# Optimization experiments

Hardware: AMD Instinct MI355X
Metric: run time of the kernel (lower is better)

## Reference

```python
import jax, jax.numpy as jnp
import numpy as np

LOG_CLAMP = -100.0  # torch.nn.BCELoss clamps log terms at -100


def setup_inputs() -> dict:
    key = jax.random.key(0)
    k1, k2 = jax.random.split(key)
    shape = (64, 8, 65536, 1)  # [B, C, H, W]
    vertical_pred = jax.random.uniform(k1, shape, dtype=jnp.float32)
    vertical_true = jax.random.uniform(k2, shape, dtype=jnp.float32)
    return {"vertical_pred": vertical_pred, "vertical_true": vertical_true}


def reference(vertical_pred, vertical_true):
    # Only the first width column is used: [B, C, H]
    p = vertical_pred[..., 0]
    t = vertical_true[..., 0]
    log_p = jnp.clip(jnp.log(p), LOG_CLAMP)
    log_1mp = jnp.clip(jnp.log1p(-p), LOG_CLAMP)
    bce = -(t * log_p + (1.0 - t) * log_1mp)           # [B, C, H]
    per_bc = jnp.mean(bce, axis=-1)                     # mean over H per (b, c)
    loss = jnp.sum(per_bc) / vertical_pred.shape[0]     # sum over b,c then / B
    return loss
```

## Files before the change

kernel.cpp:

```cpp
#include <hip/hip_runtime.h>


#define LOG2_CLAMP -144.26950408889634f

typedef float vfloat4 __attribute__((ext_vector_type(4)));

__device__ __forceinline__ void bce4_acc(vfloat4 p, vfloat4 t,
                                         float& sq, float& sd) {
    float lp, lq;
    lp = fmaxf(__log2f(p.x), LOG2_CLAMP);
    lq = fmaxf(__log2f(1.0f - p.x), LOG2_CLAMP);
    sq += lq; sd = __builtin_fmaf(t.x, lp - lq, sd);
    lp = fmaxf(__log2f(p.y), LOG2_CLAMP);
    lq = fmaxf(__log2f(1.0f - p.y), LOG2_CLAMP);
    sq += lq; sd = __builtin_fmaf(t.y, lp - lq, sd);
    lp = fmaxf(__log2f(p.z), LOG2_CLAMP);
    lq = fmaxf(__log2f(1.0f - p.z), LOG2_CLAMP);
    sq += lq; sd = __builtin_fmaf(t.z, lp - lq, sd);
    lp = fmaxf(__log2f(p.w), LOG2_CLAMP);
    lq = fmaxf(__log2f(1.0f - p.w), LOG2_CLAMP);
    sq += lq; sd = __builtin_fmaf(t.w, lp - lq, sd);
}

__global__ __launch_bounds__(256) void vertical_loss_kernel(
    const vfloat4* __restrict__ p4,
    const vfloat4* __restrict__ t4,
    float* __restrict__ out,
    int n4, float final_scale)
{
    float sq = 0.0f, sd = 0.0f;

    const int chunk = n4 / (int)gridDim.x;
    const int steps = chunk / (int)blockDim.x;

    if ((chunk % (int)blockDim.x) == 0 && steps > 0) {
        const int stp = (int)blockDim.x;
        int i = (int)blockIdx.x * chunk + (int)threadIdx.x;
        #pragma unroll 4
        for (int s = 0; s < steps; ++s, i += stp) {
            vfloat4 p = __builtin_nontemporal_load(&p4[i]);
            vfloat4 t = __builtin_nontemporal_load(&t4[i]);
            bce4_acc(p, t, sq, sd);
        }
    } else {
        for (int i = (int)blockIdx.x * (int)blockDim.x + (int)threadIdx.x;
             i < n4; i += (int)gridDim.x * (int)blockDim.x) {
            vfloat4 p = __builtin_nontemporal_load(&p4[i]);
            vfloat4 t = __builtin_nontemporal_load(&t4[i]);
            bce4_acc(p, t, sq, sd);
        }
    }

    float sum = sq + sd;

    #pragma unroll
    for (int off = 32; off > 0; off >>= 1)
        sum += __shfl_down(sum, off, 64);

    __shared__ float wsum[4];
    int wave = threadIdx.x >> 6;
    int lane = threadIdx.x & 63;
    if (lane == 0) wsum[wave] = sum;
    __syncthreads();

    if (threadIdx.x == 0) {
        float s = wsum[0] + wsum[1] + wsum[2] + wsum[3];
        atomicAdd(out, s * final_scale);
    }
}

extern "C" void kernel_launch(void* const* d_in, const int* in_sizes, int n_in,
                              void* d_out, int out_size, void* d_ws, size_t ws_size,
                              hipStream_t stream) {
    const vfloat4* pred  = (const vfloat4*)d_in[0];
    const vfloat4* true_ = (const vfloat4*)d_in[1];
    float* out = (float*)d_out;

    int n  = in_sizes[0];
    int n4 = n / 4;
    float final_scale = -0.69314718055994531f / (65536.0f * 64.0f);

    (void)hipMemsetAsync(d_out, 0, sizeof(float), stream);

    int blocks = 2048;
    vertical_loss_kernel<<<blocks, 256, 0, stream>>>(pred, true_, out, n4, final_scale);
}
```

Baseline: 254.5 us.

## Software-pipeline loads with inline asm cache-bypass global loads and explicit waitcnt

Replaces the unrolled nontemporal-load loop with a hand-written double-buffered pipeline. Each iteration issues inline-asm global_load_dwordx4 with sc0 sc1 nt cache-bypass bits and uses explicit s_waitcnt plus sched barriers, so two iterations of loads stay in flight while the math runs. The aim is better memory-level parallelism and less cache pollution on a purely bandwidth-bound stream. In exchange, it may keep fewer loads outstanding than the compiler's unroll-by-4, and the unsigned 32-bit byte offsets limit how large the inputs can be.

```diff
diff --git a/kernel.cpp b/kernel.cpp
--- a/kernel.cpp
+++ b/kernel.cpp
@@ -22,9 +22,23 @@
     sq += lq; sd = __builtin_fmaf(t.w, lp - lq, sd);
 }
 
+__device__ __forceinline__ vfloat4 ld_bypass(const float* __restrict__ base,
+                                             unsigned byte_off) {
+    vfloat4 r;
+    asm volatile("global_load_dwordx4 %0, %1, %2 sc0 sc1 nt"
+                 : "=v"(r)
+                 : "v"(byte_off), "s"(base));
+    return r;
+}
+
+#define WAITCNT(n) do {                                            \
+        asm volatile("s_waitcnt vmcnt(" #n ")" ::: "memory");      \
+        __builtin_amdgcn_sched_barrier(0);                         \
+    } while (0)
+
 __global__ __launch_bounds__(256) void vertical_loss_kernel(
-    const vfloat4* __restrict__ p4,
-    const vfloat4* __restrict__ t4,
+    const float* __restrict__ pf,
+    const float* __restrict__ tf,
     float* __restrict__ out,
     int n4, float final_scale)
 {
@@ -33,16 +47,41 @@
     const int chunk = n4 / (int)gridDim.x;
     const int steps = chunk / (int)blockDim.x;
 
-    if ((chunk % (int)blockDim.x) == 0 && steps > 0) {
-        const int stp = (int)blockDim.x;
-        int i = (int)blockIdx.x * chunk + (int)threadIdx.x;
-        #pragma unroll 4
-        for (int s = 0; s < steps; ++s, i += stp) {
-            vfloat4 p = __builtin_nontemporal_load(&p4[i]);
-            vfloat4 t = __builtin_nontemporal_load(&t4[i]);
-            bce4_acc(p, t, sq, sd);
+    const bool fast = ((n4 % (int)gridDim.x) == 0) &&
+                      ((chunk % (int)blockDim.x) == 0) &&
+                      (steps >= 2) && ((steps & 1) == 0);
+
+    if (fast) {
+        const unsigned stride = (unsigned)blockDim.x * 16u;
+        unsigned off = ((unsigned)blockIdx.x * (unsigned)chunk +
+                        threadIdx.x) * 16u;
+
+        vfloat4 pA = ld_bypass(pf, off);
+        vfloat4 tA = ld_bypass(tf, off);
+        vfloat4 pB = ld_bypass(pf, off + stride);
+        vfloat4 tB = ld_bypass(tf, off + stride);
+        unsigned offI = off + 2u * stride;
+
+        int s = 0;
+        for (; s + 4 <= steps; s += 2) {
+            WAITCNT(2);
+            bce4_acc(pA, tA, sq, sd);
+            pA = ld_bypass(pf, offI);
+            tA = ld_bypass(tf, offI);
+            offI += stride;
+            WAITCNT(2);
+            bce4_acc(pB, tB, sq, sd);
+            pB = ld_bypass(pf, offI);
+            tB = ld_bypass(tf, offI);
+            offI += stride;
         }
+        WAITCNT(2);
+        bce4_acc(pA, tA, sq, sd);
+        WAITCNT(0);
+        bce4_acc(pB, tB, sq, sd);
     } else {
+        const vfloat4* p4 = (const vfloat4*)pf;
+        const vfloat4* t4 = (const vfloat4*)tf;
         for (int i = (int)blockIdx.x * (int)blockDim.x + (int)threadIdx.x;
              i < n4; i += (int)gridDim.x * (int)blockDim.x) {
             vfloat4 p = __builtin_nontemporal_load(&p4[i]);
@@ -64,16 +103,16 @@
     __syncthreads();
 
     if (threadIdx.x == 0) {
-        float s = wsum[0] + wsum[1] + wsum[2] + wsum[3];
-        atomicAdd(out, s * final_scale);
+        float fs = wsum[0] + wsum[1] + wsum[2] + wsum[3];
+        atomicAdd(out, fs * final_scale);
     }
 }
 
 extern "C" void kernel_launch(void* const* d_in, const int* in_sizes, int n_in,
                               void* d_out, int out_size, void* d_ws, size_t ws_size,
                               hipStream_t stream) {
-    const vfloat4* pred  = (const vfloat4*)d_in[0];
-    const vfloat4* true_ = (const vfloat4*)d_in[1];
+    const float* pred  = (const float*)d_in[0];
+    const float* true_ = (const float*)d_in[1];
     float* out = (float*)d_out;
 
     int n  = in_sizes[0];
```

New measurement: 255.7 us. Within noise of the previous version (+0.5%).
